# Kernel tuning notes

Measured on AMD Instinct MI355X. Metric: run time of the kernel, lower is better.

## Reference

```python
import jax, jax.numpy as jnp
import numpy as np

S, B, L = 512, 256, 128  # seq_length, batch_size, label_nums
PAD_ID, START_ID = 0, 1


def setup_inputs() -> dict:
    key = jax.random.key(0)
    k1, k2, k3, k4 = jax.random.split(key, 4)
    emit_scores = jax.random.normal(k1, (S, B, L), dtype=jnp.float32)
    labels = jax.random.randint(k2, (B, S), 0, L, dtype=jnp.int32)
    # contiguous prefix masks: lengths in [1, S]
    lengths = jax.random.randint(k3, (B,), 1, S + 1, dtype=jnp.int32)
    masks = jnp.arange(S, dtype=jnp.int32)[None, :] < lengths[:, None]  # (B, S) bool
    T = jax.random.normal(k4, (L, L), dtype=jnp.float32) * 0.1  # transition params
    return {"emit_scores": emit_scores, "labels": labels, "masks": masks, "T": T}


def reference(emit_scores, labels, masks, T):
    seq_len, batch, label_nums = emit_scores.shape

    # ---- gold path score (calc_sentences_scores) ----
    lengths = masks.astype(jnp.int32).sum(axis=1)                       # (B,)
    ends_index = jnp.take_along_axis(labels, (lengths - 1)[:, None], axis=1)[:, 0]
    ends_scores = T[ends_index, PAD_ID].sum()

    labels_ext = jnp.concatenate(
        [jnp.full((batch, 1), START_ID, dtype=labels.dtype), labels], axis=1)  # (B, S+1)
    prev = labels_ext[:, :-1]                                           # (B, S)
    nxt = labels                                                        # (B, S)
    emit_bt = jnp.transpose(emit_scores, (1, 0, 2))                     # (B, S, L)
    emit_sel = jnp.take_along_axis(emit_bt, nxt[:, :, None], axis=2)[:, :, 0]  # (B, S)
    trans_sel = T[prev, nxt]                                            # (B, S)
    gold = jnp.where(masks, emit_sel + trans_sel, 0.0).sum() + ends_scores

    # ---- partition function (crf_encode): log-sum-exp scan over time ----
    fs0 = emit_scores[0] + T[START_ID][None, :]                         # (B, L)

    def step(fs, inp):
        e_t, m_t = inp                                                  # (B, L), (B,)
        # scores[b, i, j] = fs[b, i] + T[i, j] + e_t[b, j]
        scores = fs[:, :, None] + T[None, :, :] + e_t[:, None, :]
        cur = jax.nn.logsumexp(scores, axis=1)                          # (B, L)
        fs = jnp.where(m_t[:, None], cur, fs)
        return fs, None

    fs, _ = jax.lax.scan(step, fs0, (emit_scores[1:], masks.T[1:]))
    encode = jax.nn.logsumexp(fs + T[:, PAD_ID][None, :], axis=1).sum()

    return encode - gold
```

## Files before the change

### kernel.cpp

```cpp
#include <hip/hip_runtime.h>
#include <hip/hip_fp8.h>

#define S_LEN 512
#define BATCH 256
#define L 128
#define PAD_ID 0
#define START_ID 1

typedef int    i32x8 __attribute__((ext_vector_type(8)));
typedef int    i32x4 __attribute__((ext_vector_type(4)));
typedef float  f32x4 __attribute__((ext_vector_type(4)));
typedef unsigned int   u32x4 __attribute__((ext_vector_type(4)));
typedef unsigned short u16x2 __attribute__((ext_vector_type(2)));

__device__ __forceinline__ unsigned int umax2(unsigned int a, unsigned int b) {
    u16x2 x = __builtin_bit_cast(u16x2, a), y = __builtin_bit_cast(u16x2, b);
#if defined(__has_builtin) && __has_builtin(__builtin_elementwise_max)
    return __builtin_bit_cast(unsigned int, __builtin_elementwise_max(x, y));
#else
    u16x2 r; r.x = x.x > y.x ? x.x : y.x; r.y = x.y > y.y ? x.y : y.y;
    return __builtin_bit_cast(unsigned int, r);
#endif
}
__device__ __forceinline__ float frcp(float x) {
#if defined(__has_builtin) && __has_builtin(__builtin_amdgcn_rcpf)
    return __builtin_amdgcn_rcpf(x);
#else
    return 1.0f / x;
#endif
}
__device__ __forceinline__ unsigned short f2bf(float f) {
    unsigned int u = __builtin_bit_cast(unsigned int, f);
    return (unsigned short)((u + 0x7fffu + ((u >> 16) & 1u)) >> 16);
}
__device__ __forceinline__ float bf2f(unsigned short b) {
    return __builtin_bit_cast(float, (unsigned int)b << 16);
}
__device__ __forceinline__ float sane(float x, float lo, float hi) {
    return fminf(fmaxf(x, lo), hi);
}
__device__ __forceinline__ int pk2_fp8(float a, float b) {
#if defined(__has_builtin) && __has_builtin(__builtin_amdgcn_cvt_pk_fp8_f32)
    return __builtin_amdgcn_cvt_pk_fp8_f32(a, b, 0, false);
#else
    __hip_fp8_e4m3 A(a), B(b);
    return (int)A.__x | ((int)B.__x << 8);
#endif
}
__device__ __forceinline__ unsigned int bmax8(u32x4 a, u32x4 b) {
    const unsigned int M = 0x00FF00FFu;
    unsigned int l0 = umax2(a.x & M, a.y & M), l1 = umax2(a.z & M, a.w & M);
    unsigned int l2 = umax2(b.x & M, b.y & M), l3 = umax2(b.z & M, b.w & M);
    unsigned int h0 = umax2((a.x >> 8) & M, (a.y >> 8) & M);
    unsigned int h1 = umax2((a.z >> 8) & M, (a.w >> 8) & M);
    unsigned int h2 = umax2((b.x >> 8) & M, (b.y >> 8) & M);
    unsigned int h3 = umax2((b.z >> 8) & M, (b.w >> 8) & M);
    unsigned int v = umax2(umax2(umax2(l0, l1), umax2(l2, l3)),
                           umax2(umax2(h0, h1), umax2(h2, h3)));
    u16x2 t = __builtin_bit_cast(u16x2, v);
    return (unsigned int)(t.x > t.y ? t.x : t.y);
}
__device__ __forceinline__ float fp8dec(unsigned int bb) {
    bb &= 0x7Fu;
    int e = (int)(bb >> 3), mt = (int)(bb & 7u);
    float v = e ? __builtin_ldexpf((float)(8 + mt), e - 10)
                : __builtin_ldexpf((float)mt, -9);
    return sane(v, 1e-9f, 448.f);
}

#define WS_QF 0
#define WS_QB 32768
#define WS_SF 65536
#define WS_SB 66560
#define WS_N  67584

__global__ __launch_bounds__(256, 1) void k_scan2(
        const float* __restrict__ emit, const int* __restrict__ labels,
        const void* __restrict__ masks, const float* __restrict__ T,
        unsigned char* __restrict__ ws, float* __restrict__ out) {
    const int b   = blockIdx.x & (BATCH - 1);
    const int dir = blockIdx.x >> 8;
    const int tid = threadIdx.x;
    const int w = tid >> 6;
    const int lane = tid & 63;
    const int g = lane >> 4, m = lane & 15;
    const int ja = 32 * w + m, jb = ja + 16;

    __shared__ unsigned short elds[255][L];
    __shared__ __align__(16) unsigned char qs[2][L];
    __shared__ __align__(8)  unsigned char hb[2][4];
    __shared__ float part[4];
    __shared__ float fsx[4];
    __shared__ int   ib[4];

    {
        const unsigned int* mw0 = (const unsigned int*)masks;
        int pred = 0;
        #pragma unroll
        for (int k = 0; k < 8; ++k) {
            unsigned int w0 = mw0[tid + 256 * k];
            pred |= (w0 > 1u && w0 != 0x3f800000u);
        }
        unsigned long long bal = __ballot(pred);
        if (lane == 0) ib[w] = (bal != 0ull) ? 1 : 0;
        if (tid < 8)   ((unsigned char*)hb)[tid] = 0x38;
        if (tid < 256) ((unsigned char*)qs)[tid] = 0x38;
        if (tid < 4)   { part[tid] = 0.f; fsx[tid] = 0.f; }
    }
    __syncthreads();
    const bool isbyte = (ib[0] | ib[1] | ib[2] | ib[3]) != 0;

    int len;
    {
        int cnt = 0;
        if (isbyte) {
            const unsigned int* mw = (const unsigned int*)masks + b * (S_LEN / 4);
            #pragma unroll
            for (int k = 0; k < 2; ++k) {
                unsigned int w0 = mw[lane + 64 * k];
                cnt += ((w0 & 0xffu) != 0) + ((w0 & 0xff00u) != 0) +
                       ((w0 & 0xff0000u) != 0) + ((w0 & 0xff000000u) != 0);
            }
        } else {
            const unsigned int* mw = (const unsigned int*)masks + b * S_LEN;
            #pragma unroll
            for (int k = 0; k < 8; ++k) cnt += (mw[lane + 64 * k] != 0u);
        }
        #pragma unroll
        for (int off = 32; off; off >>= 1) cnt += __shfl_xor(cnt, off, 64);
        len = cnt;
    }
    const int n  = len - 1;
    const int kf = n / 2;
    const int nB = n - kf - 1;
    const int steps = dir ? (nB > 0 ? nB : 0) : kf;

#define LDBX(BF, nt, TR)                                                                     \
    {                                                                                        \
        _Pragma("unroll")                                                                    \
        for (int d = 0; d < 8; ++d) {                                                        \
            int s0 = 32 * g + 4 * d;                                                         \
            float v0, v1, v2, v3;                                                            \
            if (TR) {                                                                        \
                v0 = __expf(T[(16 * (nt) + m) * L + (16 * ((s0 + 0) & 7) + ((s0 + 0) >> 3))]); \
                v1 = __expf(T[(16 * (nt) + m) * L + (16 * ((s0 + 1) & 7) + ((s0 + 1) >> 3))]); \
                v2 = __expf(T[(16 * (nt) + m) * L + (16 * ((s0 + 2) & 7) + ((s0 + 2) >> 3))]); \
                v3 = __expf(T[(16 * (nt) + m) * L + (16 * ((s0 + 3) & 7) + ((s0 + 3) >> 3))]); \
            } else {                                                                         \
                v0 = __expf(T[(16 * ((s0 + 0) & 7) + ((s0 + 0) >> 3)) * L + 16 * (nt) + m]);   \
                v1 = __expf(T[(16 * ((s0 + 1) & 7) + ((s0 + 1) >> 3)) * L + 16 * (nt) + m]);   \
                v2 = __expf(T[(16 * ((s0 + 2) & 7) + ((s0 + 2) >> 3)) * L + 16 * (nt) + m]);   \
                v3 = __expf(T[(16 * ((s0 + 3) & 7) + ((s0 + 3) >> 3)) * L + 16 * (nt) + m]);   \
            }                                                                                \
            int p01 = pk2_fp8(v0, v1), p23 = pk2_fp8(v2, v3);                                \
            BF[d] = (p01 & 0xffff) | (p23 << 16);                                            \
        }                                                                                    \
    }
    i32x8 Bq0, Bq1;
    if (dir == 0) { LDBX(Bq0, 2 * w, 0) LDBX(Bq1, 2 * w + 1, 0) }
    else          { LDBX(Bq0, 2 * w, 1) LDBX(Bq1, 2 * w + 1, 1) }

    for (int idx = tid; idx < steps * 64; idx += 256) {
        int rl = idx >> 6, c2 = (idx & 63) * 2;
        int row = dir ? (kf + 1 + rl) : (1 + rl);
        const float* ep = emit + ((size_t)row * BATCH + b) * L + c2;
        float e0 = ep[0], e1 = ep[1];
        *(unsigned int*)&elds[rl][c2] =
            (unsigned int)f2bf(e0) | ((unsigned int)f2bf(e1) << 16);
    }

    float fa = 0.f, fbv = 0.f;
    const bool active = (dir == 0) || (n >= 1);
    if (dir == 0) {
        fa  = emit[b * L + ja] + T[START_ID * L + ja];
        fbv = emit[b * L + jb] + T[START_ID * L + jb];
    } else if (n >= 1) {
        fa  = emit[((size_t)n * BATCH + b) * L + ja] + T[ja * L + PAD_ID];
        fbv = emit[((size_t)n * BATCH + b) * L + jb] + T[jb * L + PAD_ID];
    }
    {
        float mx = fmaxf(fa, fbv);
        #pragma unroll
        for (int off = 32; off; off >>= 1) mx = fmaxf(mx, __shfl_xor(mx, off, 64));
        if (lane == 0) fsx[w] = mx;
    }
    __syncthreads();
    float S = 0.f, p0 = 0.f, p1 = 0.f;
    if (active) {
        S = fmaxf(fmaxf(fsx[0], fsx[1]), fmaxf(fsx[2], fsx[3]));
        p0 = sane(__expf(fa - S), 1e-9f, 400.f);
        p1 = sane(__expf(fbv - S), 1e-9f, 400.f);
        if (g == 0)
            *(short*)&qs[0][8 * m + 2 * w] = (short)(pk2_fp8(p0, p1) & 0xffff);
    }
    __syncthreads();

    const f32x4 z = {0.f, 0.f, 0.f, 0.f};
    for (int i = 0; i < steps; ++i) {
        const int rb = i & 1, wb2 = (i + 1) & 1;
        const int slot = dir ? (nB - 1 - i) : i;

        i32x4 alo = *(const i32x4*)&qs[rb][32 * g];
        i32x4 ahi = *(const i32x4*)&qs[rb][32 * g + 16];
        unsigned int hd = *(const unsigned int*)&hb[rb][0];
        float ea = bf2f(elds[slot][ja]);
        float eb = bf2f(elds[slot][jb]);
        float xe0 = __expf(ea), xe1 = __expf(eb);

        {
            const unsigned int M = 0x00FF00FFu;
            unsigned int v = umax2(hd & M, (hd >> 8) & M);
            u16x2 tv = __builtin_bit_cast(u16x2, v);
            hd = (unsigned int)(tv.x > tv.y ? tv.x : tv.y);
        }
        float msc = fp8dec(hd);
        float kk = frcp(msc);

        i32x8 A;
        A[0] = alo[0]; A[1] = alo[1]; A[2] = alo[2]; A[3] = alo[3];
        A[4] = ahi[0]; A[5] = ahi[1]; A[6] = ahi[2]; A[7] = ahi[3];

        f32x4 c0 = __builtin_amdgcn_mfma_scale_f32_16x16x128_f8f6f4(A, Bq0, z, 0, 0, 0, 127, 0, 127);
        f32x4 c1 = __builtin_amdgcn_mfma_scale_f32_16x16x128_f8f6f4(A, Bq1, z, 0, 0, 0, 127, 0, 127);

        unsigned int qm = bmax8(__builtin_bit_cast(u32x4, alo),
                                __builtin_bit_cast(u32x4, ahi));
        if (w == 0 && m == 0) hb[wb2][g] = (unsigned char)(qm & 0x7Fu);

        p0 = sane(c0[0] * kk * xe0, 1e-9f, 400.f);
        p1 = sane(c1[0] * kk * xe1, 1e-9f, 400.f);
        if (g == 0)
            *(short*)&qs[wb2][8 * m + 2 * w] = (short)(pk2_fp8(p0, p1) & 0xffff);
        S += __logf(msc);
        __syncthreads();
    }

    unsigned char* seam = ws + (dir ? WS_QB : WS_QF) + b * L;
    if (tid < 32) ((int*)seam)[tid] = ((const int*)qs[steps & 1])[tid];
    if (tid == 0) {
        ((float*)(ws + (dir ? WS_SB : WS_SF)))[b] = S;
        if (dir == 0) ((int*)(ws + WS_N))[b] = n;
    }

    if (dir == 0) {
        float gsum = 0.f;
        for (int tt = tid; tt < len; tt += 256) {
            int nxt = labels[b * S_LEN + tt];
            int prv = tt ? labels[b * S_LEN + tt - 1] : START_ID;
            gsum += emit[((size_t)tt * BATCH + b) * L + nxt] + T[prv * L + nxt];
            if (tt == len - 1) gsum += T[nxt * L + PAD_ID];
        }
        #pragma unroll
        for (int off = 32; off; off >>= 1) gsum += __shfl_xor(gsum, off, 64);
        if (lane == 0) part[w] = gsum;
        __syncthreads();
        if (tid == 0)
            atomicAdd(out, -((part[0] + part[1]) + (part[2] + part[3])));
    }
}

__global__ __launch_bounds__(64, 1) void k_join(
        const float* __restrict__ T, const unsigned char* __restrict__ ws,
        float* __restrict__ out) {
    const int b = blockIdx.x;
    const int lane = threadIdx.x;
    __shared__ float qsh[L], ush[L];

    const int n = ((const int*)(ws + WS_N))[b];
    #pragma unroll
    for (int k = 0; k < 2; ++k) {
        int s = lane + 64 * k;
        int j = 16 * (s & 7) + (s >> 3);
        qsh[j] = fp8dec(ws[WS_QF + b * L + s]);
        ush[j] = fp8dec(ws[WS_QB + b * L + s]);
    }
    __syncthreads();

    float ev = 0.f;
    if (n >= 1) {
        #pragma unroll
        for (int k = 0; k < 2; ++k) {
            int j = lane + 64 * k;
            float v = 0.f;
            for (int i = 0; i < L; ++i)
                v = fmaf(qsh[i], __expf(T[i * L + j]), v);
            ev += v * ush[j];
        }
    } else {
        #pragma unroll
        for (int k = 0; k < 2; ++k) {
            int j = lane + 64 * k;
            ev += qsh[j] * __expf(T[j * L + PAD_ID]);
        }
    }
    #pragma unroll
    for (int off = 32; off; off >>= 1) ev += __shfl_xor(ev, off, 64);

    if (lane == 0) {
        float Sf = ((const float*)(ws + WS_SF))[b];
        float Sb = (n >= 1) ? ((const float*)(ws + WS_SB))[b] : 0.f;
        float enc = Sf + Sb + __logf(fmaxf(ev, 1e-35f));
        atomicAdd(out, sane(enc, -1e30f, 1e30f));
    }
}

extern "C" void kernel_launch(void* const* d_in, const int* in_sizes, int n_in,
                              void* d_out, int out_size, void* d_ws, size_t ws_size,
                              hipStream_t stream) {
    const float* emit   = (const float*)d_in[0];
    const int*   labels = (const int*)d_in[1];
    const void*  masks  = d_in[2];
    const float* T      = (const float*)d_in[3];
    float* out = (float*)d_out;
    unsigned char* ws = (unsigned char*)d_ws;

    hipMemsetAsync(d_out, 0, sizeof(float), stream);
    k_scan2<<<dim3(2 * BATCH), dim3(256), 0, stream>>>(emit, labels, masks, T, ws, out);
    k_join <<<dim3(BATCH),     dim3(64),  0, stream>>>(T, ws, out);
}
```

Before: 229.6 us.

## Run each CRF scan direction in a single wavefront with register-resident transition matrix

Rewrites the bidirectional forward scan so each batch/direction is handled by one 64-lane wavefront instead of four waves. The whole exp(T) fp8 matrix is held in registers as eight MFMA operands, and the per-step scale reduction uses lane shuffles, so the per-step __syncthreads barrier goes away. Emission rows are prefetched from global memory four steps ahead instead of being staged into a bf16 LDS buffer first. The gold-path score moves into extra dedicated blocks. The cost is eight MFMAs per step on one wave instead of two per wave, plus high register pressure.

```diff
diff --git a/kernel.cpp b/kernel.cpp
--- a/kernel.cpp
+++ b/kernel.cpp
@@ -28,13 +28,6 @@
 #else
     return 1.0f / x;
 #endif
-}
-__device__ __forceinline__ unsigned short f2bf(float f) {
-    unsigned int u = __builtin_bit_cast(unsigned int, f);
-    return (unsigned short)((u + 0x7fffu + ((u >> 16) & 1u)) >> 16);
-}
-__device__ __forceinline__ float bf2f(unsigned short b) {
-    return __builtin_bit_cast(float, (unsigned int)b << 16);
 }
 __device__ __forceinline__ float sane(float x, float lo, float hi) {
     return fminf(fmaxf(x, lo), hi);
@@ -74,188 +67,196 @@
 #define WS_SB 66560
 #define WS_N  67584
 
-__global__ __launch_bounds__(256, 1) void k_scan2(
+__device__ __forceinline__ int compute_len(const void* masks, int b, int lane) {
+    const unsigned int* mw0 = (const unsigned int*)masks;
+    int pred = 0;
+    #pragma unroll
+    for (int k = 0; k < 32; ++k) {
+        unsigned int w0 = mw0[lane + 64 * k];
+        pred |= (w0 > 1u && w0 != 0x3f800000u);
+    }
+    const bool isbyte = (__ballot(pred) != 0ull);
+    int cnt = 0;
+    if (isbyte) {
+        const unsigned int* mw = mw0 + b * (S_LEN / 4);
+        #pragma unroll
+        for (int k = 0; k < 2; ++k) {
+            unsigned int w0 = mw[lane + 64 * k];
+            cnt += ((w0 & 0xffu) != 0) + ((w0 & 0xff00u) != 0) +
+                   ((w0 & 0xff0000u) != 0) + ((w0 & 0xff000000u) != 0);
+        }
+    } else {
+        const unsigned int* mw = mw0 + b * S_LEN;
+        #pragma unroll
+        for (int k = 0; k < 8; ++k) cnt += (mw[lane + 64 * k] != 0u);
+    }
+    #pragma unroll
+    for (int off = 32; off; off >>= 1) cnt += __shfl_xor(cnt, off, 64);
+    return cnt;
+}
+
+__global__ __launch_bounds__(64, 1) void k_scan(
         const float* __restrict__ emit, const int* __restrict__ labels,
         const void* __restrict__ masks, const float* __restrict__ T,
         unsigned char* __restrict__ ws, float* __restrict__ out) {
-    const int b   = blockIdx.x & (BATCH - 1);
-    const int dir = blockIdx.x >> 8;
-    const int tid = threadIdx.x;
-    const int w = tid >> 6;
-    const int lane = tid & 63;
+    const int bid  = blockIdx.x;
+    const int lane = threadIdx.x;
+
+    if (bid >= 2 * BATCH) {
+        const int b = bid - 2 * BATCH;
+        const int len = compute_len(masks, b, lane);
+        float gsum = 0.f;
+        for (int tt = lane; tt < len; tt += 64) {
+            int nxt = labels[b * S_LEN + tt];
+            int prv = tt ? labels[b * S_LEN + tt - 1] : START_ID;
+            gsum += emit[((size_t)tt * BATCH + b) * L + nxt] + T[prv * L + nxt];
+            if (tt == len - 1) gsum += T[nxt * L + PAD_ID];
+        }
+        #pragma unroll
+        for (int off = 32; off; off >>= 1) gsum += __shfl_xor(gsum, off, 64);
+        if (lane == 0) atomicAdd(out, -gsum);
+        return;
+    }
+
+    const int b   = bid & (BATCH - 1);
+    const int dir = bid >> 8;
     const int g = lane >> 4, m = lane & 15;
-    const int ja = 32 * w + m, jb = ja + 16;
-
-    __shared__ unsigned short elds[255][L];
-    __shared__ __align__(16) unsigned char qs[2][L];
-    __shared__ __align__(8)  unsigned char hb[2][4];
-    __shared__ float part[4];
-    __shared__ float fsx[4];
-    __shared__ int   ib[4];
-
-    {
-        const unsigned int* mw0 = (const unsigned int*)masks;
-        int pred = 0;
-        #pragma unroll
-        for (int k = 0; k < 8; ++k) {
-            unsigned int w0 = mw0[tid + 256 * k];
-            pred |= (w0 > 1u && w0 != 0x3f800000u);
-        }
-        unsigned long long bal = __ballot(pred);
-        if (lane == 0) ib[w] = (bal != 0ull) ? 1 : 0;
-        if (tid < 8)   ((unsigned char*)hb)[tid] = 0x38;
-        if (tid < 256) ((unsigned char*)qs)[tid] = 0x38;
-        if (tid < 4)   { part[tid] = 0.f; fsx[tid] = 0.f; }
-    }
-    __syncthreads();
-    const bool isbyte = (ib[0] | ib[1] | ib[2] | ib[3]) != 0;
-
-    int len;
-    {
-        int cnt = 0;
-        if (isbyte) {
-            const unsigned int* mw = (const unsigned int*)masks + b * (S_LEN / 4);
-            #pragma unroll
-            for (int k = 0; k < 2; ++k) {
-                unsigned int w0 = mw[lane + 64 * k];
-                cnt += ((w0 & 0xffu) != 0) + ((w0 & 0xff00u) != 0) +
-                       ((w0 & 0xff0000u) != 0) + ((w0 & 0xff000000u) != 0);
-            }
-        } else {
-            const unsigned int* mw = (const unsigned int*)masks + b * S_LEN;
-            #pragma unroll
-            for (int k = 0; k < 8; ++k) cnt += (mw[lane + 64 * k] != 0u);
-        }
-        #pragma unroll
-        for (int off = 32; off; off >>= 1) cnt += __shfl_xor(cnt, off, 64);
-        len = cnt;
-    }
+
+    const int len = compute_len(masks, b, lane);
     const int n  = len - 1;
     const int kf = n / 2;
     const int nB = n - kf - 1;
     const int steps = dir ? (nB > 0 ? nB : 0) : kf;
-
-#define LDBX(BF, nt, TR)                                                                     \
-    {                                                                                        \
-        _Pragma("unroll")                                                                    \
-        for (int d = 0; d < 8; ++d) {                                                        \
-            int s0 = 32 * g + 4 * d;                                                         \
-            float v0, v1, v2, v3;                                                            \
-            if (TR) {                                                                        \
-                v0 = __expf(T[(16 * (nt) + m) * L + (16 * ((s0 + 0) & 7) + ((s0 + 0) >> 3))]); \
-                v1 = __expf(T[(16 * (nt) + m) * L + (16 * ((s0 + 1) & 7) + ((s0 + 1) >> 3))]); \
-                v2 = __expf(T[(16 * (nt) + m) * L + (16 * ((s0 + 2) & 7) + ((s0 + 2) >> 3))]); \
-                v3 = __expf(T[(16 * (nt) + m) * L + (16 * ((s0 + 3) & 7) + ((s0 + 3) >> 3))]); \
-            } else {                                                                         \
-                v0 = __expf(T[(16 * ((s0 + 0) & 7) + ((s0 + 0) >> 3)) * L + 16 * (nt) + m]);   \
-                v1 = __expf(T[(16 * ((s0 + 1) & 7) + ((s0 + 1) >> 3)) * L + 16 * (nt) + m]);   \
-                v2 = __expf(T[(16 * ((s0 + 2) & 7) + ((s0 + 2) >> 3)) * L + 16 * (nt) + m]);   \
-                v3 = __expf(T[(16 * ((s0 + 3) & 7) + ((s0 + 3) >> 3)) * L + 16 * (nt) + m]);   \
-            }                                                                                \
-            int p01 = pk2_fp8(v0, v1), p23 = pk2_fp8(v2, v3);                                \
-            BF[d] = (p01 & 0xffff) | (p23 << 16);                                            \
-        }                                                                                    \
-    }
-    i32x8 Bq0, Bq1;
-    if (dir == 0) { LDBX(Bq0, 2 * w, 0) LDBX(Bq1, 2 * w + 1, 0) }
-    else          { LDBX(Bq0, 2 * w, 1) LDBX(Bq1, 2 * w + 1, 1) }
-
-    for (int idx = tid; idx < steps * 64; idx += 256) {
-        int rl = idx >> 6, c2 = (idx & 63) * 2;
-        int row = dir ? (kf + 1 + rl) : (1 + rl);
-        const float* ep = emit + ((size_t)row * BATCH + b) * L + c2;
-        float e0 = ep[0], e1 = ep[1];
-        *(unsigned int*)&elds[rl][c2] =
-            (unsigned int)f2bf(e0) | ((unsigned int)f2bf(e1) << 16);
-    }
-
-    float fa = 0.f, fbv = 0.f;
-    const bool active = (dir == 0) || (n >= 1);
+    if (dir == 1 && n < 1) return;
+
+    const int tm = m >> 1;
+    const int j1 = 16 * tm + 4 * g + 2 * (m & 1);
+    const int s1 = 8 * (j1 & 15) + tm;
+
+    __shared__ __align__(16) unsigned char st[128];
+
+    i32x8 Af[8];
+    #pragma unroll
+    for (int t = 0; t < 8; ++t) {
+        #pragma unroll
+        for (int d = 0; d < 8; ++d) {
+            float v[4];
+            #pragma unroll
+            for (int y = 0; y < 4; ++y) {
+                int sl = 4 * d + y;
+                int k  = 16 * (sl & 7) + 4 * g + (sl >> 3);
+                int idx = dir ? ((16 * t + m) * L + k) : (k * L + 16 * t + m);
+                v[y] = __expf(T[idx]);
+            }
+            int p01 = pk2_fp8(v[0], v[1]), p23 = pk2_fp8(v[2], v[3]);
+            Af[t][d] = (p01 & 0xffff) | (p23 << 16);
+        }
+    }
+
+    float f1, f2;
     if (dir == 0) {
-        fa  = emit[b * L + ja] + T[START_ID * L + ja];
-        fbv = emit[b * L + jb] + T[START_ID * L + jb];
-    } else if (n >= 1) {
-        fa  = emit[((size_t)n * BATCH + b) * L + ja] + T[ja * L + PAD_ID];
-        fbv = emit[((size_t)n * BATCH + b) * L + jb] + T[jb * L + PAD_ID];
-    }
+        f1 = emit[(size_t)b * L + j1]     + T[START_ID * L + j1];
+        f2 = emit[(size_t)b * L + j1 + 1] + T[START_ID * L + j1 + 1];
+    } else {
+        const float* er = emit + ((size_t)n * BATCH + b) * L;
+        f1 = er[j1]     + T[j1 * L + PAD_ID];
+        f2 = er[j1 + 1] + T[(j1 + 1) * L + PAD_ID];
+    }
+    float S;
     {
-        float mx = fmaxf(fa, fbv);
+        float mx = fmaxf(f1, f2);
         #pragma unroll
         for (int off = 32; off; off >>= 1) mx = fmaxf(mx, __shfl_xor(mx, off, 64));
-        if (lane == 0) fsx[w] = mx;
-    }
-    __syncthreads();
-    float S = 0.f, p0 = 0.f, p1 = 0.f;
-    if (active) {
-        S = fmaxf(fmaxf(fsx[0], fsx[1]), fmaxf(fsx[2], fsx[3]));
-        p0 = sane(__expf(fa - S), 1e-9f, 400.f);
-        p1 = sane(__expf(fbv - S), 1e-9f, 400.f);
-        if (g == 0)
-            *(short*)&qs[0][8 * m + 2 * w] = (short)(pk2_fp8(p0, p1) & 0xffff);
-    }
-    __syncthreads();
+        S = mx;
+    }
+    {
+        float p0 = sane(__expf(f1 - S), 1e-9f, 400.f);
+        float p1 = sane(__expf(f2 - S), 1e-9f, 400.f);
+        int pk = pk2_fp8(p0, p1);
+        st[s1]     = (unsigned char)(pk & 0xff);
+        st[s1 + 8] = (unsigned char)((pk >> 8) & 0xff);
+    }
+    asm volatile("s_waitcnt lgkmcnt(0)" ::: "memory");
+    i32x4 alo = *(const i32x4*)&st[32 * g];
+    i32x4 ahi = *(const i32x4*)&st[32 * g + 16];
 
     const f32x4 z = {0.f, 0.f, 0.f, 0.f};
-    for (int i = 0; i < steps; ++i) {
-        const int rb = i & 1, wb2 = (i + 1) & 1;
-        const int slot = dir ? (nB - 1 - i) : i;
-
-        i32x4 alo = *(const i32x4*)&qs[rb][32 * g];
-        i32x4 ahi = *(const i32x4*)&qs[rb][32 * g + 16];
-        unsigned int hd = *(const unsigned int*)&hb[rb][0];
-        float ea = bf2f(elds[slot][ja]);
-        float eb = bf2f(elds[slot][jb]);
-        float xe0 = __expf(ea), xe1 = __expf(eb);
-
-        {
-            const unsigned int M = 0x00FF00FFu;
-            unsigned int v = umax2(hd & M, (hd >> 8) & M);
-            u16x2 tv = __builtin_bit_cast(u16x2, v);
-            hd = (unsigned int)(tv.x > tv.y ? tv.x : tv.y);
-        }
-        float msc = fp8dec(hd);
-        float kk = frcp(msc);
-
-        i32x8 A;
-        A[0] = alo[0]; A[1] = alo[1]; A[2] = alo[2]; A[3] = alo[3];
-        A[4] = ahi[0]; A[5] = ahi[1]; A[6] = ahi[2]; A[7] = ahi[3];
-
-        f32x4 c0 = __builtin_amdgcn_mfma_scale_f32_16x16x128_f8f6f4(A, Bq0, z, 0, 0, 0, 127, 0, 127);
-        f32x4 c1 = __builtin_amdgcn_mfma_scale_f32_16x16x128_f8f6f4(A, Bq1, z, 0, 0, 0, 127, 0, 127);
-
-        unsigned int qm = bmax8(__builtin_bit_cast(u32x4, alo),
-                                __builtin_bit_cast(u32x4, ahi));
-        if (w == 0 && m == 0) hb[wb2][g] = (unsigned char)(qm & 0x7Fu);
-
-        p0 = sane(c0[0] * kk * xe0, 1e-9f, 400.f);
-        p1 = sane(c1[0] * kk * xe1, 1e-9f, 400.f);
-        if (g == 0)
-            *(short*)&qs[wb2][8 * m + 2 * w] = (short)(pk2_fp8(p0, p1) & 0xffff);
-        S += __logf(msc);
-        __syncthreads();
-    }
-
-    unsigned char* seam = ws + (dir ? WS_QB : WS_QF) + b * L;
-    if (tid < 32) ((int*)seam)[tid] = ((const int*)qs[steps & 1])[tid];
-    if (tid == 0) {
+    const int base1 = b * L + j1;
+
+    if (steps > 0) {
+        auto ldrow = [&](int idx) -> float2 {
+            int ii  = idx < steps - 1 ? idx : steps - 1;
+            int row = dir ? (n - 1 - ii) : (1 + ii);
+            return *(const float2*)(emit + (size_t)row * (BATCH * L) + base1);
+        };
+        float2 eb0 = ldrow(0), eb1 = ldrow(1), eb2 = ldrow(2), eb3 = ldrow(3);
+        int i = 0;
+
+#define MFS(AT) __builtin_amdgcn_mfma_scale_f32_16x16x128_f8f6f4((AT), Aq, z, 0, 0, 0, 127, 0, 127)
+#define STEP(EB)                                                               \
+        {                                                                      \
+            i32x8 Aq;                                                          \
+            Aq[0] = alo[0]; Aq[1] = alo[1]; Aq[2] = alo[2]; Aq[3] = alo[3];    \
+            Aq[4] = ahi[0]; Aq[5] = ahi[1]; Aq[6] = ahi[2]; Aq[7] = ahi[3];    \
+            f32x4 d0 = MFS(Af[0]), d1 = MFS(Af[1]), d2 = MFS(Af[2]),           \
+                  d3 = MFS(Af[3]), d4 = MFS(Af[4]), d5 = MFS(Af[5]),           \
+                  d6 = MFS(Af[6]), d7 = MFS(Af[7]);                            \
+            unsigned int qm = bmax8(__builtin_bit_cast(u32x4, alo),            \
+                                    __builtin_bit_cast(u32x4, ahi));           \
+            {                                                                  \
+                unsigned int q2 = (unsigned int)__shfl_xor((int)qm, 16, 64);   \
+                qm = qm > q2 ? qm : q2;                                        \
+                q2 = (unsigned int)__shfl_xor((int)qm, 32, 64);                \
+                qm = qm > q2 ? qm : q2;                                        \
+            }                                                                  \
+            float msc = fp8dec(qm);                                            \
+            float kk  = frcp(msc);                                             \
+            float xe0 = __expf(EB.x) * kk, xe1 = __expf(EB.y) * kk;            \
+            const bool sr = (m & 1) != 0, sB = (m & 2) != 0,                   \
+                       sC = (m & 4) != 0, sD = (m & 8) != 0;                   \
+            float a0 = sr ? d0[2] : d0[0], b0 = sr ? d0[3] : d0[1];            \
+            float a1 = sr ? d1[2] : d1[0], b1 = sr ? d1[3] : d1[1];            \
+            float a2 = sr ? d2[2] : d2[0], b2 = sr ? d2[3] : d2[1];            \
+            float a3 = sr ? d3[2] : d3[0], b3 = sr ? d3[3] : d3[1];            \
+            float a4 = sr ? d4[2] : d4[0], b4 = sr ? d4[3] : d4[1];            \
+            float a5 = sr ? d5[2] : d5[0], b5 = sr ? d5[3] : d5[1];            \
+            float a6 = sr ? d6[2] : d6[0], b6 = sr ? d6[3] : d6[1];            \
+            float a7 = sr ? d7[2] : d7[0], b7 = sr ? d7[3] : d7[1];            \
+            float aA = sB ? a1 : a0, aB2 = sB ? a3 : a2;                       \
+            float aC = sB ? a5 : a4, aD2 = sB ? a7 : a6;                       \
+            float bA = sB ? b1 : b0, bB2 = sB ? b3 : b2;                       \
+            float bC = sB ? b5 : b4, bD2 = sB ? b7 : b6;                       \
+            float aE = sC ? aB2 : aA, aF = sC ? aD2 : aC;                      \
+            float bE = sC ? bB2 : bA, bF = sC ? bD2 : bC;                      \
+            float c0 = sD ? aF : aE, c1 = sD ? bF : bE;                        \
+            float p0 = sane(c0 * xe0, 1e-9f, 400.f);                           \
+            float p1 = sane(c1 * xe1, 1e-9f, 400.f);                           \
+            int pk = pk2_fp8(p0, p1);                                          \
+            st[s1]     = (unsigned char)(pk & 0xff);                           \
+            st[s1 + 8] = (unsigned char)((pk >> 8) & 0xff);                    \
+            asm volatile("s_waitcnt lgkmcnt(0)" ::: "memory");                 \
+            alo = *(const i32x4*)&st[32 * g];                                  \
+            ahi = *(const i32x4*)&st[32 * g + 16];                             \
+            S += __logf(msc);                                                  \
+        }
+
+        for (;;) {
+            STEP(eb0); eb0 = ldrow(i + 4); if (++i == steps) break;
+            STEP(eb1); eb1 = ldrow(i + 4); if (++i == steps) break;
+            STEP(eb2); eb2 = ldrow(i + 4); if (++i == steps) break;
+            STEP(eb3); eb3 = ldrow(i + 4); if (++i == steps) break;
+        }
+#undef STEP
+#undef MFS
+    }
+
+    if (m == 0) {
+        i32x4* sp = (i32x4*)(ws + (dir ? WS_QB : WS_QF) + b * L + 32 * g);
+        sp[0] = alo; sp[1] = ahi;
+    }
+    if (lane == 0) {
         ((float*)(ws + (dir ? WS_SB : WS_SF)))[b] = S;
         if (dir == 0) ((int*)(ws + WS_N))[b] = n;
-    }
-
-    if (dir == 0) {
-        float gsum = 0.f;
-        for (int tt = tid; tt < len; tt += 256) {
-            int nxt = labels[b * S_LEN + tt];
-            int prv = tt ? labels[b * S_LEN + tt - 1] : START_ID;
-            gsum += emit[((size_t)tt * BATCH + b) * L + nxt] + T[prv * L + nxt];
-            if (tt == len - 1) gsum += T[nxt * L + PAD_ID];
-        }
-        #pragma unroll
-        for (int off = 32; off; off >>= 1) gsum += __shfl_xor(gsum, off, 64);
-        if (lane == 0) part[w] = gsum;
-        __syncthreads();
-        if (tid == 0)
-            atomicAdd(out, -((part[0] + part[1]) + (part[2] + part[3])));
     }
 }
 
@@ -315,6 +316,6 @@
     unsigned char* ws = (unsigned char*)d_ws;
 
     hipMemsetAsync(d_out, 0, sizeof(float), stream);
-    k_scan2<<<dim3(2 * BATCH), dim3(256), 0, stream>>>(emit, labels, masks, T, ws, out);
-    k_join <<<dim3(BATCH),     dim3(64),  0, stream>>>(T, ws, out);
-}
+    k_scan<<<dim3(3 * BATCH), dim3(64), 0, stream>>>(emit, labels, masks, T, ws, out);
+    k_join<<<dim3(BATCH),     dim3(64), 0, stream>>>(T, ws, out);
+}
```

New measurement: 247.3 us. 7.7% more time.
